# Kernel optimization log

Hardware: AMD Instinct MI355X
Metric: run time of the kernel (lower is better)

Reference implementation:

```python
import jax, jax.numpy as jnp
import numpy as np

P1 = np.array([[1000.0, 0.0, 128.0, 64000.0],
               [0.0, 1000.0, 128.0, 64000.0],
               [0.0, 0.0, 1.0, 500.0]])
P2 = np.array([[-128.0, 0.0, 1000.0, 64000.0],
               [-128.0, 1000.0, 0.0, 64000.0],
               [-1.0, 0.0, 0.0, 500.0]])


def calculate_fundamental_matrix(P_src, P_dst):
    # l2 = F21 @ x1 : maps a point in P_src onto a line in P_dst
    C1 = -np.linalg.inv(P_src[:3, :3]) @ P_src[:3, 3]
    e = P_dst @ np.append(C1, 1.0)          # epipole of src camera center in dst view
    return np.cross(e, np.eye(3) * -1) @ P_dst @ np.linalg.pinv(P_src)


def setup_inputs() -> dict:
    key = jax.random.key(0)
    view1 = jax.random.normal(key, (8, 4, 256, 256), dtype=jnp.float32)
    F21 = calculate_fundamental_matrix(P1, P2).astype(np.float32)
    return {"view1": view1, "F": jnp.asarray(F21)}


def reference(view1, F):
    """Epipolar image translation: out(x2) = line integral of view1 along the
    epipolar line l1 = F^T @ x2 (bilinear sampling in v, unit steps in u,
    zero outside the image). Matches fume_torch_lib.translate semantics."""
    B, C, H, W = view1.shape
    dt = view1.dtype
    F = F.astype(dt)
    ys = jnp.arange(H, dtype=dt)[:, None]   # (H,1)
    xs = jnp.arange(W, dtype=dt)[None, :]   # (1,W)
    # line coefficients l = F^T @ [x, y, 1], per output pixel -> (H,W)
    a = F[0, 0] * xs + F[1, 0] * ys + F[2, 0]
    b = F[0, 1] * xs + F[1, 1] * ys + F[2, 1]
    c = F[0, 2] * xs + F[1, 2] * ys + F[2, 2]
    n = jnp.sqrt(a * a + b * b) + jnp.asarray(1e-12, dt)
    a, b, c = a / n, b / n, c / n
    ok = (jnp.abs(b) > 1e-6).astype(dt)                 # drop near-vertical lines
    b_safe = jnp.where(jnp.abs(b) > 1e-6, b, jnp.asarray(1.0, dt))

    def step(acc, u):
        uf = u.astype(dt)
        v = -(a * uf + c) / b_safe                      # (H,W) source row per out pixel
        v0 = jnp.floor(v)
        f = v - v0
        i0 = v0.astype(jnp.int32)
        i1 = i0 + 1
        m0 = ((i0 >= 0) & (i0 < H)).astype(dt)
        m1 = ((i1 >= 0) & (i1 < H)).astype(dt)
        col = jax.lax.dynamic_index_in_dim(view1, u, axis=3, keepdims=False)  # (B,C,H)
        s0 = col[:, :, jnp.clip(i0, 0, H - 1)]          # (B,C,H,W)
        s1 = col[:, :, jnp.clip(i1, 0, H - 1)]
        val = (s0 * (1.0 - f) * m0 + s1 * f * m1) * ok
        return acc + val, None

    out, _ = jax.lax.scan(step, jnp.zeros_like(view1), jnp.arange(W))
    return out
```

## Files before the change

kernel.cpp:

```cpp
#include <hip/hip_runtime.h>
#include <cstdint>

constexpr int Hh = 256, Ww = 256, BCc = 32;
constexpr int RBLK = 35;
constexpr int USTRIDE = RBLK * BCc * 8 * 2;
constexpr int UPLANES = 264;

typedef _Float16 half2v   __attribute__((ext_vector_type(2)));
typedef _Float16 half8v   __attribute__((ext_vector_type(8)));
typedef __fp16   fp16x2   __attribute__((ext_vector_type(2)));
typedef float    float16v __attribute__((ext_vector_type(16)));
typedef uint32_t uint4v   __attribute__((ext_vector_type(4)));

static __device__ inline half2v pack2(float a, float b) {
    fp16x2 r = __builtin_amdgcn_cvt_pkrtz(a, b);
    return __builtin_bit_cast(half2v, r);
}

__global__ __launch_bounds__(256) void fume_pack(const float* __restrict__ in,
                                                 char* __restrict__ T4) {
    const int t   = threadIdx.x;
    const int bid = blockIdx.x;
    if (bid >= 512) {
        constexpr int NA = UPLANES * 3 * 32;
        constexpr int NB = 8 * 32 * 32;
        for (int id = (bid - 512) * 256 + t; id < NA + NB; id += 8 * 256) {
            int u, blk, ch;
            if (id < NA) {
                u = id / 96;
                int rem = id - u * 96;
                int bsel = rem >> 5;
                blk = (bsel == 0) ? 0 : (bsel == 1 ? 33 : 34);
                ch = rem & 31;
            } else {
                int id2 = id - NA;
                u = 256 + (id2 >> 10);
                int rem = id2 & 1023;
                blk = 1 + (rem >> 5);
                ch = rem & 31;
            }
            uint4v z = {0, 0, 0, 0};
            *(uint4v*)(T4 + (size_t)u * USTRIDE + blk * 512 + ch * 16) = z;
        }
        return;
    }
    __shared__ float lds[8][8][65];
    const int chg = bid & 3;
    const int r0  = ((bid >> 2) & 31) * 8;
    const int u0  = (bid >> 7) * 64;
    const int blk = (r0 >> 3) + 1;

#pragma unroll
    for (int it = 0; it < 16; ++it) {
        int idx = it * 256 + t;
        int ch = idx >> 9, rr = (idx >> 6) & 7, uu = idx & 63;
        lds[ch][rr][uu] =
            in[(chg * 8 + ch) * (Hh * Ww) + (r0 + rr) * Ww + u0 + uu];
    }
    __syncthreads();
    const int chl = t & 7;
#pragma unroll
    for (int p = 0; p < 2; ++p) {
        int u_l = (t >> 3) + p * 32;
        uint32_t w[4];
#pragma unroll
        for (int j = 0; j < 4; ++j) {
            half2v pr = pack2(lds[chl][2 * j][u_l], lds[chl][2 * j + 1][u_l]);
            __builtin_memcpy(&w[j], &pr, 4);
        }
        uint4v val = {w[0], w[1], w[2], w[3]};
        *(uint4v*)(T4 + (size_t)(u0 + u_l) * USTRIDE + blk * 512
                   + (chg * 8 + chl) * 16) = val;
    }
}

__global__ __launch_bounds__(256, 4) void fume_mfma(const char* __restrict__ T4,
                                                    const float* __restrict__ Fm,
                                                    float* __restrict__ out) {
    __shared__ float red[4][32][33];
    const int t    = threadIdx.x;
    const int lane = t & 63;
    const int wq   = t >> 6;
    const int px   = lane & 31;
    const int h    = lane >> 5;
    const int bid  = (int)blockIdx.x;
    const int idx8 = bid >> 3;
    const int y    = ((bid & 7) << 5) + (idx8 >> 3);
    const int x0   = (idx8 & 7) * 32;
    const int x    = x0 + px;

    float xf = (float)x, yf = (float)y;
    float a = Fm[0] * xf + Fm[3] * yf + Fm[6];
    float b = Fm[1] * xf + Fm[4] * yf + Fm[7];
    float c = Fm[2] * xf + Fm[5] * yf + Fm[8];
    float n = sqrtf(a * a + b * b) + 1e-12f;
    a /= n; b /= n; c /= n;

    float alpha, beta_i;
    int u_lo, u_hi;
    if (fabsf(b) > 1e-6f) {
        alpha  = -a / b;
        beta_i = -c / b + 8.f;
        u_lo = 0; u_hi = Ww - 1;
        if (fabsf(alpha) > 1e-12f) {
            float inv = 1.f / alpha;
            float t0 = (7.f - beta_i) * inv;
            float t1 = (264.f - beta_i) * inv;
            int lo = (int)floorf(fminf(t0, t1));
            int hi = (int)ceilf (fmaxf(t0, t1));
            u_lo = lo > 0 ? lo : 0;
            u_hi = hi < (Ww - 1) ? hi : (Ww - 1);
        } else if (beta_i <= 7.f || beta_i >= 264.f) {
            u_lo = 1 << 20; u_hi = -(1 << 20);
        }
    } else {
        alpha = 0.f; beta_i = 3.0e4f;
        u_lo = 1 << 20; u_hi = -(1 << 20);
    }

    float xA = (float)x0, xB = (float)(x0 + 31);
    float aA = Fm[0] * xA + Fm[3] * yf + Fm[6];
    float bA = Fm[1] * xA + Fm[4] * yf + Fm[7];
    float cA = Fm[2] * xA + Fm[5] * yf + Fm[8];
    float aB = Fm[0] * xB + Fm[3] * yf + Fm[6];
    float bB = Fm[1] * xB + Fm[4] * yf + Fm[7];
    float cB = Fm[2] * xB + Fm[5] * yf + Fm[8];
    float alA = -aA / bA, beA = -cA / bA + 8.f;
    float alB = -aB / bB, beB = -cB / bB + 8.f;

    int lo = u_lo, hi = u_hi;
#pragma unroll
    for (int off = 1; off < 64; off <<= 1) {
        int l2 = __shfl_xor(lo, off, 64);
        int h2 = __shfl_xor(hi, off, 64);
        lo = lo < l2 ? lo : l2;
        hi = hi > h2 ? hi : h2;
    }
    lo = __builtin_amdgcn_readfirstlane(lo);
    hi = __builtin_amdgcn_readfirstlane(hi);

    float16v acc = {0.f, 0.f, 0.f, 0.f, 0.f, 0.f, 0.f, 0.f,
                    0.f, 0.f, 0.f, 0.f, 0.f, 0.f, 0.f, 0.f};

    if (lo <= hi) {
        int len = hi - lo + 1;
        int C   = (len + 3) >> 2;
        int cq  = (C + 3) >> 2;
        int nit = C - wq * cq;
        nit = nit < 0 ? 0 : (nit > cq ? cq : nit);
        int n4  = nit << 2;
        int us  = lo + wq * cq * 4;

        float uf  = (float)(us + lane);
        float vAl = fmaf(alA, uf, beA);
        float vBl = fmaf(alB, uf, beB);
        float mnu = fminf(vAl, vBl);
        float Mf  = floorf(fmaf(mnu, 0.125f, -0.125f));
        Mf = fmaxf(0.f, fminf(Mf, 33.f));
        int   vMo  = (int)Mf << 9;
        float vB8f = Mf * 8.f;
        int   vB8i = __builtin_bit_cast(int, vB8f);

        float l8h = (float)(8 * h);
        float vh  = fmaf(alpha, (float)us, beta_i) - l8h;
        const char* pb  = T4 + (size_t)us * USTRIDE;
        const int voff  = (h << 9) + (px << 4);

        const half2v one2 = {(_Float16)1.f, (_Float16)1.f};

        for (int it2 = 0; it2 < n4; it2 += 4) {
#pragma unroll
            for (int i = 0; i < 4; ++i) {
                const int idx = it2 + i;
                int   Mo = __builtin_amdgcn_readlane(vMo, idx);
                float b8 = __builtin_bit_cast(
                    float, __builtin_amdgcn_readlane(vB8i, idx));
                uint4v bw = *(const uint4v*)(pb + (size_t)idx * USTRIDE
                                             + (size_t)Mo + voff);

                float vbl = vh - b8;
                half2v vb2 = pack2(vbl, vbl);
                uint32_t aw[4];
#pragma unroll
                for (int j = 0; j < 4; ++j) {
                    half2v cj = {(_Float16)(float)(2 * j),
                                 (_Float16)(float)(2 * j + 1)};
                    half2v d  = vb2 - cj;
                    uint32_t du;
                    __builtin_memcpy(&du, &d, 4);
                    du &= 0x7fff7fffu;
                    half2v ad;
                    __builtin_memcpy(&ad, &du, 4);
                    half2v tj;
                    asm("v_pk_add_f16 %0, %1, %2 neg_lo:[0,1] neg_hi:[0,1] clamp"
                        : "=v"(tj)
                        : "v"(one2), "v"(ad));
                    __builtin_memcpy(&aw[j], &tj, 4);
                }
                half8v A;
                __builtin_memcpy(&A, aw, 16);
                half8v B = __builtin_bit_cast(half8v, bw);
                acc = __builtin_amdgcn_mfma_f32_32x32x16_f16(A, B, acc, 0, 0, 0);

                vh += alpha;
            }
        }
    }

#pragma unroll
    for (int r = 0; r < 16; ++r) {
        int m = (r & 3) + 8 * (r >> 2) + 4 * h;
        red[wq][m][px] = acc[r];
    }
    __syncthreads();
    {
        int pxs = t & 31, cg = t >> 5;
#pragma unroll
        for (int jj = 0; jj < 4; ++jj) {
            int ch = cg + 8 * jj;
            float val = red[0][pxs][ch] + red[1][pxs][ch]
                      + red[2][pxs][ch] + red[3][pxs][ch];
            out[(size_t)ch * (Hh * Ww) + y * Ww + x0 + pxs] = val;
        }
    }
}

__global__ __launch_bounds__(256) void fume_fallback(const float* __restrict__ src,
                                                     const float* __restrict__ Fm,
                                                     float* __restrict__ out) {
    int g = blockIdx.x * 256 + threadIdx.x;
    int part = g & 3;
    int pix  = g >> 2;
    int x = pix & (Ww - 1);
    int y = pix >> 8;
    int ch0 = part * 8;
    float xf = (float)x, yf = (float)y;
    float a = Fm[0] * xf + Fm[3] * yf + Fm[6];
    float b = Fm[1] * xf + Fm[4] * yf + Fm[7];
    float c = Fm[2] * xf + Fm[5] * yf + Fm[8];
    float n = sqrtf(a * a + b * b) + 1e-12f;
    a /= n; b /= n; c /= n;
    float acc[8];
#pragma unroll
    for (int k = 0; k < 8; ++k) acc[k] = 0.f;
    if (fabsf(b) > 1e-6f) {
        float alpha = -a / b, beta = -c / b;
        for (int u = 0; u < Ww; ++u) {
            float v  = fmaf(alpha, (float)u, beta);
            float rf = floorf(v);
            float f  = v - rf;
            int   ri = (int)rf;
            float w0 = ((unsigned)ri       < (unsigned)Hh) ? (1.f - f) : 0.f;
            float w1 = ((unsigned)(ri + 1) < (unsigned)Hh) ? f         : 0.f;
            int r0 = ri < 0 ? 0 : (ri > Hh - 1 ? Hh - 1 : ri);
            int r1 = ri + 1 < 0 ? 0 : (ri + 1 > Hh - 1 ? Hh - 1 : ri + 1);
#pragma unroll
            for (int k = 0; k < 8; ++k) {
                float s0 = src[(size_t)(ch0 + k) * (Hh * Ww) + r0 * Ww + u];
                float s1 = src[(size_t)(ch0 + k) * (Hh * Ww) + r1 * Ww + u];
                acc[k] = fmaf(w0, s0, fmaf(w1, s1, acc[k]));
            }
        }
    }
#pragma unroll
    for (int k = 0; k < 8; ++k)
        out[(size_t)(ch0 + k) * (Hh * Ww) + pix] = acc[k];
}

extern "C" void kernel_launch(void* const* d_in, const int* in_sizes, int n_in,
                              void* d_out, int out_size, void* d_ws, size_t ws_size,
                              hipStream_t stream) {
    const float* view1 = (const float*)d_in[0];
    const float* Fm    = (const float*)d_in[1];
    float* out = (float*)d_out;

    constexpr size_t t4_bytes = (size_t)UPLANES * USTRIDE;
    if (ws_size >= t4_bytes) {
        char* T4 = (char*)d_ws;
        fume_pack<<<520, 256, 0, stream>>>(view1, T4);
        fume_mfma<<<2048, 256, 0, stream>>>(T4, Fm, out);
    } else {
        fume_fallback<<<(Hh * Ww * 4) / 256, 256, 0, stream>>>(view1, Fm, out);
    }
}
```

Before: 92.33 us.

## Switch to 16x16x32 MFMA with 16-pixel tiles and two u-steps per instruction

Replaces the 32x32x16 MFMA over 32 output pixels with a pair of 16x16x32 MFMAs covering 16 pixels each, where each MFMA's K dimension spans two u-steps. The two channel halves go to separate accumulators. Per-step row offsets are now fetched with ds_bpermute instead of readlane, and the grid doubles to 4096 blocks. The intent is a tighter u-range per narrower pixel tile, less wasted K work, and more blocks for occupancy. In exchange, each block does more bpermute and load overhead and the reduction is smaller per block.

```diff
diff --git a/kernel.cpp b/kernel.cpp
--- a/kernel.cpp
+++ b/kernel.cpp
@@ -9,7 +9,7 @@
 typedef _Float16 half2v   __attribute__((ext_vector_type(2)));
 typedef _Float16 half8v   __attribute__((ext_vector_type(8)));
 typedef __fp16   fp16x2   __attribute__((ext_vector_type(2)));
-typedef float    float16v __attribute__((ext_vector_type(16)));
+typedef float    float4v  __attribute__((ext_vector_type(4)));
 typedef uint32_t uint4v   __attribute__((ext_vector_type(4)));
 
 static __device__ inline half2v pack2(float a, float b) {
@@ -77,16 +77,17 @@
 __global__ __launch_bounds__(256, 4) void fume_mfma(const char* __restrict__ T4,
                                                     const float* __restrict__ Fm,
                                                     float* __restrict__ out) {
-    __shared__ float red[4][32][33];
+    __shared__ float red[4][16][33];
     const int t    = threadIdx.x;
     const int lane = t & 63;
     const int wq   = t >> 6;
-    const int px   = lane & 31;
-    const int h    = lane >> 5;
+    const int px   = lane & 15;
+    const int h2   = (lane >> 4) & 1;
+    const int hu   = lane >> 5;
     const int bid  = (int)blockIdx.x;
     const int idx8 = bid >> 3;
-    const int y    = ((bid & 7) << 5) + (idx8 >> 3);
-    const int x0   = (idx8 & 7) * 32;
+    const int y    = ((bid & 7) << 5) + (idx8 >> 4);
+    const int x0   = (idx8 & 15) * 16;
     const int x    = x0 + px;
 
     float xf = (float)x, yf = (float)y;
@@ -118,7 +119,7 @@
         u_lo = 1 << 20; u_hi = -(1 << 20);
     }
 
-    float xA = (float)x0, xB = (float)(x0 + 31);
+    float xA = (float)x0, xB = (float)(x0 + 15);
     float aA = Fm[0] * xA + Fm[3] * yf + Fm[6];
     float bA = Fm[1] * xA + Fm[4] * yf + Fm[7];
     float cA = Fm[2] * xA + Fm[5] * yf + Fm[8];
@@ -132,15 +133,15 @@
 #pragma unroll
     for (int off = 1; off < 64; off <<= 1) {
         int l2 = __shfl_xor(lo, off, 64);
-        int h2 = __shfl_xor(hi, off, 64);
+        int h2x = __shfl_xor(hi, off, 64);
         lo = lo < l2 ? lo : l2;
-        hi = hi > h2 ? hi : h2;
+        hi = hi > h2x ? hi : h2x;
     }
     lo = __builtin_amdgcn_readfirstlane(lo);
     hi = __builtin_amdgcn_readfirstlane(hi);
 
-    float16v acc = {0.f, 0.f, 0.f, 0.f, 0.f, 0.f, 0.f, 0.f,
-                    0.f, 0.f, 0.f, 0.f, 0.f, 0.f, 0.f, 0.f};
+    float4v acc0 = {0.f, 0.f, 0.f, 0.f};
+    float4v acc1 = {0.f, 0.f, 0.f, 0.f};
 
     if (lo <= hi) {
         int len = hi - lo + 1;
@@ -161,22 +162,27 @@
         float vB8f = Mf * 8.f;
         int   vB8i = __builtin_bit_cast(int, vB8f);
 
-        float l8h = (float)(8 * h);
-        float vh  = fmaf(alpha, (float)us, beta_i) - l8h;
-        const char* pb  = T4 + (size_t)us * USTRIDE;
-        const int voff  = (h << 9) + (px << 4);
+        float alpha2 = alpha + alpha;
+        float vh = fmaf(alpha, (float)(us + hu), beta_i) - (float)(8 * h2);
+        const char* pb = T4 + (size_t)us * USTRIDE;
+        const int voffc = hu * USTRIDE + (h2 << 9) + (px << 4);
+        const int hu4   = hu << 2;
 
         const half2v one2 = {(_Float16)1.f, (_Float16)1.f};
 
-        for (int it2 = 0; it2 < n4; it2 += 4) {
-#pragma unroll
-            for (int i = 0; i < 4; ++i) {
-                const int idx = it2 + i;
-                int   Mo = __builtin_amdgcn_readlane(vMo, idx);
+        int niter = n4 >> 1;
+        for (int it2 = 0; it2 < niter; it2 += 2) {
+#pragma unroll
+            for (int i = 0; i < 2; ++i) {
+                const int itc = it2 + i;
+                int pa  = hu4 + (itc << 3);
+                int Mo  = __builtin_amdgcn_ds_bpermute(pa, vMo);
                 float b8 = __builtin_bit_cast(
-                    float, __builtin_amdgcn_readlane(vB8i, idx));
-                uint4v bw = *(const uint4v*)(pb + (size_t)idx * USTRIDE
-                                             + (size_t)Mo + voff);
+                    float, __builtin_amdgcn_ds_bpermute(pa, vB8i));
+                const char* q = pb + (size_t)itc * (2 * USTRIDE)
+                              + (size_t)(Mo + voffc);
+                uint4v bw0 = *(const uint4v*)(q);
+                uint4v bw1 = *(const uint4v*)(q + 256);
 
                 float vbl = vh - b8;
                 half2v vb2 = pack2(vbl, vbl);
@@ -199,29 +205,32 @@
                 }
                 half8v A;
                 __builtin_memcpy(&A, aw, 16);
-                half8v B = __builtin_bit_cast(half8v, bw);
-                acc = __builtin_amdgcn_mfma_f32_32x32x16_f16(A, B, acc, 0, 0, 0);
-
-                vh += alpha;
+                half8v B0 = __builtin_bit_cast(half8v, bw0);
+                half8v B1 = __builtin_bit_cast(half8v, bw1);
+                acc0 = __builtin_amdgcn_mfma_f32_16x16x32_f16(A, B0, acc0,
+                                                              0, 0, 0);
+                acc1 = __builtin_amdgcn_mfma_f32_16x16x32_f16(A, B1, acc1,
+                                                              0, 0, 0);
+                vh += alpha2;
             }
         }
     }
 
 #pragma unroll
-    for (int r = 0; r < 16; ++r) {
-        int m = (r & 3) + 8 * (r >> 2) + 4 * h;
-        red[wq][m][px] = acc[r];
+    for (int r = 0; r < 4; ++r) {
+        int m = ((lane >> 4) << 2) + r;
+        red[wq][m][lane & 15]        = acc0[r];
+        red[wq][m][(lane & 15) + 16] = acc1[r];
     }
     __syncthreads();
     {
-        int pxs = t & 31, cg = t >> 5;
-#pragma unroll
-        for (int jj = 0; jj < 4; ++jj) {
-            int ch = cg + 8 * jj;
-            float val = red[0][pxs][ch] + red[1][pxs][ch]
-                      + red[2][pxs][ch] + red[3][pxs][ch];
-            out[(size_t)ch * (Hh * Ww) + y * Ww + x0 + pxs] = val;
-        }
+        int pxs = t & 15, ch = t >> 4;
+        float v0 = red[0][pxs][ch] + red[1][pxs][ch]
+                 + red[2][pxs][ch] + red[3][pxs][ch];
+        float v1 = red[0][pxs][ch + 16] + red[1][pxs][ch + 16]
+                 + red[2][pxs][ch + 16] + red[3][pxs][ch + 16];
+        out[(size_t)ch * (Hh * Ww) + y * Ww + x0 + pxs] = v0;
+        out[(size_t)(ch + 16) * (Hh * Ww) + y * Ww + x0 + pxs] = v1;
     }
 }
 
@@ -278,7 +287,7 @@
     if (ws_size >= t4_bytes) {
         char* T4 = (char*)d_ws;
         fume_pack<<<520, 256, 0, stream>>>(view1, T4);
-        fume_mfma<<<2048, 256, 0, stream>>>(T4, Fm, out);
+        fume_mfma<<<4096, 256, 0, stream>>>(T4, Fm, out);
     } else {
         fume_fallback<<<(Hh * Ww * 4) / 256, 256, 0, stream>>>(view1, Fm, out);
     }
```

Measured after the change: 102.2 us. 10.6% more time.

## Add row-pair fp16 packed layout with per-lane window offsets and bpermute-broadcast MFMA loop

Applied to the files above, without the earlier changes.

Adds a new pack kernel that stores fp16 row pairs in two parity planes, tiled through LDS, with channels contiguous. It also adds an MFMA kernel that computes a per-u row window start (floored minimum of the line's v over the 32-pixel tile) and broadcasts offsets via ds_bpermute. The kernel does two u-steps per lane-half and loads B as four 32-bit words, replacing the readlane-driven 16-byte loads over the 35-block layout. The aim is tighter source windows and less redundant packed data, at the cost of scattered 4-byte loads and a larger workspace, with the old path kept as a fallback.

```diff
diff --git a/kernel.cpp b/kernel.cpp
--- a/kernel.cpp
+++ b/kernel.cpp
@@ -2,9 +2,15 @@
 #include <cstdint>
 
 constexpr int Hh = 256, Ww = 256, BCc = 32;
+
 constexpr int RBLK = 35;
 constexpr int USTRIDE = RBLK * BCc * 8 * 2;
 constexpr int UPLANES = 264;
+
+constexpr int DW2    = 140;
+constexpr int UROW2  = DW2 * BCc * 4;
+constexpr size_t PSIZE = (size_t)UPLANES * UROW2;
+constexpr size_t T5_BYTES = 2 * PSIZE;
 
 typedef _Float16 half2v   __attribute__((ext_vector_type(2)));
 typedef _Float16 half8v   __attribute__((ext_vector_type(8)));
@@ -15,6 +21,208 @@
 static __device__ inline half2v pack2(float a, float b) {
     fp16x2 r = __builtin_amdgcn_cvt_pkrtz(a, b);
     return __builtin_bit_cast(half2v, r);
+}
+
+__global__ __launch_bounds__(256) void fume_pack2(const float* __restrict__ in,
+                                                  char* __restrict__ P) {
+    const int t   = threadIdx.x;
+    const int bid = blockIdx.x;
+    const int rt  = bid % 18;
+    const int ut  = bid / 18;
+    const int R0  = rt * 16;
+    const int u0  = ut * 16;
+    __shared__ float lds[32][17][17];
+
+    for (int idx = t; idx < 32 * 17 * 16; idx += 256) {
+        int ch  = idx / (17 * 16);
+        int rem = idx - ch * (17 * 16);
+        int rl  = rem >> 4;
+        int uu  = rem & 15;
+        int r   = R0 + rl - 8;
+        int u   = u0 + uu;
+        float v = 0.f;
+        if ((unsigned)r < 256u && u < 256)
+            v = in[ch * (Hh * Ww) + r * Ww + u];
+        lds[ch][rl][uu] = v;
+    }
+    __syncthreads();
+
+    for (int w = t; w < 8192; w += 256) {
+        int ch    = w & 31;
+        int rest  = w >> 5;
+        int uu    = rest & 15;
+        int rest2 = rest >> 4;
+        int dd    = rest2 & 7;
+        int p     = rest2 >> 3;
+        int d     = (R0 >> 1) + dd;
+        int u     = u0 + uu;
+        if (d >= DW2 || u >= UPLANES) continue;
+        int rl = 2 * dd + p;
+        half2v pr = pack2(lds[ch][rl][uu], lds[ch][rl + 1][uu]);
+        uint32_t wv;
+        __builtin_memcpy(&wv, &pr, 4);
+        *(uint32_t*)(P + (size_t)p * PSIZE + (size_t)u * UROW2
+                     + d * 128 + ch * 4) = wv;
+    }
+}
+
+__global__ __launch_bounds__(256, 4) void fume_mfma2(const char* __restrict__ P,
+                                                     const float* __restrict__ Fm,
+                                                     float* __restrict__ out) {
+    __shared__ float red[4][32][33];
+    const int t    = threadIdx.x;
+    const int lane = t & 63;
+    const int wq   = t >> 6;
+    const int px   = lane & 31;
+    const int h    = lane >> 5;
+    const int bid  = (int)blockIdx.x;
+    const int idx8 = bid >> 3;
+    const int y    = ((bid & 7) << 5) + (idx8 >> 3);
+    const int x0   = (idx8 & 7) * 32;
+    const int x    = x0 + px;
+
+    float xf = (float)x, yf = (float)y;
+    float a = Fm[0] * xf + Fm[3] * yf + Fm[6];
+    float b = Fm[1] * xf + Fm[4] * yf + Fm[7];
+    float c = Fm[2] * xf + Fm[5] * yf + Fm[8];
+    float n = sqrtf(a * a + b * b) + 1e-12f;
+    a /= n; b /= n; c /= n;
+
+    float alpha, beta_i;
+    int u_lo, u_hi;
+    if (fabsf(b) > 1e-6f) {
+        alpha  = -a / b;
+        beta_i = -c / b + 8.f;
+        u_lo = 0; u_hi = Ww - 1;
+        if (fabsf(alpha) > 1e-12f) {
+            float inv = 1.f / alpha;
+            float t0 = (7.f - beta_i) * inv;
+            float t1 = (264.f - beta_i) * inv;
+            int lo = (int)floorf(fminf(t0, t1));
+            int hi = (int)ceilf (fmaxf(t0, t1));
+            u_lo = lo > 0 ? lo : 0;
+            u_hi = hi < (Ww - 1) ? hi : (Ww - 1);
+        } else if (beta_i <= 7.f || beta_i >= 264.f) {
+            u_lo = 1 << 20; u_hi = -(1 << 20);
+        }
+    } else {
+        alpha = 0.f; beta_i = 3.0e4f;
+        u_lo = 1 << 20; u_hi = -(1 << 20);
+    }
+
+    float xA = (float)x0, xB = (float)(x0 + 31);
+    float aA = Fm[0] * xA + Fm[3] * yf + Fm[6];
+    float bA = Fm[1] * xA + Fm[4] * yf + Fm[7];
+    float cA = Fm[2] * xA + Fm[5] * yf + Fm[8];
+    float aB = Fm[0] * xB + Fm[3] * yf + Fm[6];
+    float bB = Fm[1] * xB + Fm[4] * yf + Fm[7];
+    float cB = Fm[2] * xB + Fm[5] * yf + Fm[8];
+    float alA = -aA / bA, beA = -cA / bA + 8.f;
+    float alB = -aB / bB, beB = -cB / bB + 8.f;
+
+    int lo = u_lo, hi = u_hi;
+#pragma unroll
+    for (int off = 1; off < 64; off <<= 1) {
+        int l2 = __shfl_xor(lo, off, 64);
+        int h2 = __shfl_xor(hi, off, 64);
+        lo = lo < l2 ? lo : l2;
+        hi = hi > h2 ? hi : h2;
+    }
+    lo = __builtin_amdgcn_readfirstlane(lo);
+    hi = __builtin_amdgcn_readfirstlane(hi);
+
+    float16v acc = {0.f, 0.f, 0.f, 0.f, 0.f, 0.f, 0.f, 0.f,
+                    0.f, 0.f, 0.f, 0.f, 0.f, 0.f, 0.f, 0.f};
+
+    if (lo <= hi) {
+        int len = hi - lo + 1;
+        int C   = (len + 3) >> 2;
+        int cq  = (C + 3) >> 2;
+        int nit = C - wq * cq;
+        nit = nit < 0 ? 0 : (nit > cq ? cq : nit);
+        int npair = nit << 1;
+        int us  = lo + wq * cq * 4;
+
+        int   u_l = us + lane;
+        float uf  = (float)u_l;
+        float vAl = fmaf(alA, uf, beA);
+        float vBl = fmaf(alB, uf, beB);
+        float mnu = fminf(vAl, vBl);
+        float Mff = floorf(mnu - 0.01f);
+        Mff = fmaxf(0.f, fminf(Mff, 272.f));
+        int   Mi   = (int)Mff;
+        int   pb   = Mi & 1;
+        int   vOff = (pb ? (int)PSIZE : 0) + u_l * UROW2 + (Mi >> 1) * 128;
+        int   vMfB = __builtin_bit_cast(int, Mff);
+
+        float alpha2 = alpha + alpha;
+        float vhh = fmaf(alpha, (float)(us + h), beta_i);
+        const int h4  = h << 2;
+        const int chb = px << 2;
+
+        const half2v one2 = {(_Float16)1.f, (_Float16)1.f};
+
+#define FUME_PAIR(T)                                                          \
+    do {                                                                      \
+        int baddr = ((T) << 3) + h4;                                          \
+        int offv  = __builtin_amdgcn_ds_bpermute(baddr, vOff);                \
+        float mf  = __builtin_bit_cast(                                       \
+            float, __builtin_amdgcn_ds_bpermute(baddr, vMfB));                \
+        const char* q = P + (unsigned)(offv + chb);                           \
+        uint32_t b0 = *(const uint32_t*)(q);                                  \
+        uint32_t b1 = *(const uint32_t*)(q + 128);                            \
+        uint32_t b2 = *(const uint32_t*)(q + 256);                            \
+        uint32_t b3 = *(const uint32_t*)(q + 384);                            \
+        float vbl = vhh - mf;                                                 \
+        half2v vb2 = pack2(vbl, vbl);                                         \
+        uint32_t aw[4];                                                       \
+        _Pragma("unroll")                                                     \
+        for (int j_ = 0; j_ < 4; ++j_) {                                      \
+            half2v cj = {(_Float16)(float)(2 * j_),                           \
+                         (_Float16)(float)(2 * j_ + 1)};                      \
+            half2v d_  = vb2 - cj;                                            \
+            uint32_t du;                                                      \
+            __builtin_memcpy(&du, &d_, 4);                                    \
+            du &= 0x7fff7fffu;                                                \
+            half2v ad;                                                        \
+            __builtin_memcpy(&ad, &du, 4);                                    \
+            half2v tj;                                                        \
+            asm("v_pk_add_f16 %0, %1, %2 neg_lo:[0,1] neg_hi:[0,1] clamp"     \
+                : "=v"(tj)                                                    \
+                : "v"(one2), "v"(ad));                                        \
+            __builtin_memcpy(&aw[j_], &tj, 4);                                \
+        }                                                                     \
+        half8v A;                                                             \
+        __builtin_memcpy(&A, aw, 16);                                         \
+        uint4v bw = {b0, b1, b2, b3};                                         \
+        half8v B = __builtin_bit_cast(half8v, bw);                            \
+        acc = __builtin_amdgcn_mfma_f32_32x32x16_f16(A, B, acc, 0, 0, 0);     \
+        vhh += alpha2;                                                        \
+    } while (0)
+
+        for (int tp = 0; tp < npair; tp += 2) {
+            FUME_PAIR(tp);
+            FUME_PAIR(tp + 1);
+        }
+#undef FUME_PAIR
+    }
+
+#pragma unroll
+    for (int r = 0; r < 16; ++r) {
+        int m = (r & 3) + 8 * (r >> 2) + 4 * h;
+        red[wq][m][px] = acc[r];
+    }
+    __syncthreads();
+    {
+        int pxs = t & 31, cg = t >> 5;
+#pragma unroll
+        for (int jj = 0; jj < 4; ++jj) {
+            int ch = cg + 8 * jj;
+            float val = red[0][pxs][ch] + red[1][pxs][ch]
+                      + red[2][pxs][ch] + red[3][pxs][ch];
+            out[(size_t)ch * (Hh * Ww) + y * Ww + x0 + pxs] = val;
+        }
+    }
 }
 
 __global__ __launch_bounds__(256) void fume_pack(const float* __restrict__ in,
@@ -177,7 +385,6 @@
                     float, __builtin_amdgcn_readlane(vB8i, idx));
                 uint4v bw = *(const uint4v*)(pb + (size_t)idx * USTRIDE
                                              + (size_t)Mo + voff);
-
                 float vbl = vh - b8;
                 half2v vb2 = pack2(vbl, vbl);
                 uint32_t aw[4];
@@ -201,7 +408,6 @@
                 __builtin_memcpy(&A, aw, 16);
                 half8v B = __builtin_bit_cast(half8v, bw);
                 acc = __builtin_amdgcn_mfma_f32_32x32x16_f16(A, B, acc, 0, 0, 0);
-
                 vh += alpha;
             }
         }
@@ -275,7 +481,11 @@
     float* out = (float*)d_out;
 
     constexpr size_t t4_bytes = (size_t)UPLANES * USTRIDE;
-    if (ws_size >= t4_bytes) {
+    if (ws_size >= T5_BYTES) {
+        char* P = (char*)d_ws;
+        fume_pack2<<<306, 256, 0, stream>>>(view1, P);
+        fume_mfma2<<<2048, 256, 0, stream>>>(P, Fm, out);
+    } else if (ws_size >= t4_bytes) {
         char* T4 = (char*)d_ws;
         fume_pack<<<520, 256, 0, stream>>>(view1, T4);
         fume_mfma<<<2048, 256, 0, stream>>>(T4, Fm, out);
```

Result: slower. 97.07 us (+5.1%).
